# Kernel tuning notes

Measured on AMD Instinct MI355X. Metric: run time of the kernel, lower is better.

Reference implementation:

```python
import jax, jax.numpy as jnp
import numpy as np

DIM_IN = 1024
DIM_OUT = 1024


def setup_inputs() -> dict:
    key = jax.random.key(0)
    k1, k2, k3, k4 = jax.random.split(key, 4)
    X = jax.random.normal(k1, (4, 2048, DIM_IN), dtype=jnp.float32)
    s = 1.0 / np.sqrt(DIM_IN)
    Wq = jax.random.normal(k2, (DIM_IN, DIM_OUT), dtype=jnp.float32) * s
    Wk = jax.random.normal(k3, (DIM_IN, DIM_OUT), dtype=jnp.float32) * s
    Wv = jax.random.normal(k4, (DIM_IN, DIM_OUT), dtype=jnp.float32) * s
    return {"X": X, "Wq": Wq, "Wk": Wk, "Wv": Wv}


def reference(X, Wq, Wk, Wv):
    # X: [B, T, Din]; projections (qkv_bias=False)
    q = jnp.einsum('btd,de->bte', X, Wq)   # [B, T, Dout]
    k = jnp.einsum('btd,de->bte', X, Wk)
    v = jnp.einsum('btd,de->bte', X, Wv)
    T = X.shape[1]
    scores = jnp.einsum('bqe,bke->bqk', q, k)  # [B, T, T]
    causal = jnp.tril(jnp.ones((T, T), dtype=bool))  # mask upper triangle (future)
    scores = jnp.where(causal, scores, -jnp.inf)
    # scale=True: divide by sqrt(d); -inf stays -inf so order vs mask is irrelevant
    scores = scores / jnp.sqrt(jnp.asarray(k.shape[-1], dtype=scores.dtype))
    weights = jax.nn.softmax(scores, axis=-1)
    # dropout p=0.0 -> identity
    return jnp.einsum('bqk,bke->bqe', weights, v)
```

## Files before the change

### kernel.cpp

```cpp
#include <hip/hip_runtime.h>
#include <hip/hip_bf16.h>

typedef unsigned short u16;
typedef __bf16 bf16x8 __attribute__((ext_vector_type(8)));
typedef float f32x4 __attribute__((ext_vector_type(4)));
typedef unsigned short u16x8 __attribute__((ext_vector_type(8)));
typedef unsigned short u16x4 __attribute__((ext_vector_type(4)));

__device__ __forceinline__ float bf2f(u16 u) {
  unsigned int x = ((unsigned int)u) << 16;
  return __builtin_bit_cast(float, x);
}
__device__ __forceinline__ u16 f2bf(float f) {
  unsigned int x = __builtin_bit_cast(unsigned int, f);
  x = x + 0x7FFFu + ((x >> 16) & 1u);
  return (u16)(x >> 16);
}

__device__ __forceinline__ void gload_lds16(const u16* g, u16* l) {
  __builtin_amdgcn_global_load_lds(
      (const __attribute__((address_space(1))) unsigned int*)(unsigned long long)(uintptr_t)g,
      (__attribute__((address_space(3))) unsigned int*)(unsigned int)(uintptr_t)l,
      16, 0, 0);
}

__global__ __launch_bounds__(256) void prep_kernel(const float* __restrict__ X,
                                                   const float* __restrict__ Wq,
                                                   const float* __restrict__ Wk,
                                                   const float* __restrict__ Wv,
                                                   u16* __restrict__ Xb,
                                                   u16* __restrict__ Wt) {
  const int id = blockIdx.x;
  const int tid = threadIdx.x;
  if (id < 4096) {
    long i = ((long)id * 256 + tid) * 8;
    float4 a = *reinterpret_cast<const float4*>(X + i);
    float4 b = *reinterpret_cast<const float4*>(X + i + 4);
    u16x8 o;
    o[0] = f2bf(a.x); o[1] = f2bf(a.y); o[2] = f2bf(a.z); o[3] = f2bf(a.w);
    o[4] = f2bf(b.x); o[5] = f2bf(b.y); o[6] = f2bf(b.z); o[7] = f2bf(b.w);
    *reinterpret_cast<u16x8*>(Xb + i) = o;
    return;
  }
  __shared__ u16 t[64][72];
  const int id2 = id - 4096;
  const int z = id2 >> 8;
  const float* W = (z == 0) ? Wq : (z == 1) ? Wk : Wv;
  const float scale = (z == 0) ? (1.0f / 32.0f) : 1.0f;
  u16* out = Wt + (long)z * 1048576;
  const int c0 = (id2 & 15) * 64;
  const int r0 = ((id2 >> 4) & 15) * 64;
#pragma unroll
  for (int i = 0; i < 4; ++i) {
    int slot = tid + 256 * i;
    int lr = slot >> 4;
    int lc4 = slot & 15;
    float4 v = *reinterpret_cast<const float4*>(W + (long)(r0 + lr) * 1024 + c0 + lc4 * 4);
    t[lr][lc4 * 4 + 0] = f2bf(v.x * scale);
    t[lr][lc4 * 4 + 1] = f2bf(v.y * scale);
    t[lr][lc4 * 4 + 2] = f2bf(v.z * scale);
    t[lr][lc4 * 4 + 3] = f2bf(v.w * scale);
  }
  __syncthreads();
#pragma unroll
  for (int i = 0; i < 2; ++i) {
    int slot = tid + 256 * i;
    int orow = slot >> 3;
    int oc = slot & 7;
    u16x8 o;
#pragma unroll
    for (int j = 0; j < 8; ++j) o[j] = t[oc * 8 + j][orow];
    *reinterpret_cast<u16x8*>(out + (long)(c0 + orow) * 1024 + r0 + oc * 8) = o;
  }
}

__global__ __launch_bounds__(512, 4) void gemm_qkv(const u16* __restrict__ Xb,
                                                   const u16* __restrict__ Wt,
                                                   u16* __restrict__ Qb,
                                                   u16* __restrict__ Vt) {
  const int id = blockIdx.x;
  const int xcd = id & 7, j = id >> 3;
  const int bn = (xcd & 1) * 8 + (j & 7);
  const int bm = ((xcd >> 1) << 4) + (j >> 3);
  const int m0 = bm * 128, n0 = bn * 192;
  const int K = 1024;

  __shared__ u16 ldsA[2][8192];
  __shared__ u16 ldsB[2][12288];

  const int tid = threadIdx.x;
  const int lane = tid & 63;
  const int wid = tid >> 6;
  const int wm = wid >> 2, wn = wid & 3;
  const int l16 = lane & 15, lh = lane >> 4;
  const int strow = tid >> 3;
  const int scol = ((tid & 7) ^ (strow & 7)) * 8;
  const int rsw = l16 & 7;

  f32x4 acc[4][3];
#pragma unroll
  for (int mi = 0; mi < 4; ++mi)
#pragma unroll
    for (int ni = 0; ni < 3; ++ni) acc[mi][ni] = (f32x4)(0.0f);

  auto stage = [&](int d, int k0) {
#pragma unroll
    for (int l = 0; l < 2; ++l)
      gload_lds16(Xb + (long)(m0 + l * 64 + strow) * K + k0 + scol,
                  &ldsA[d][l * 4096 + tid * 8]);
#pragma unroll
    for (int l = 0; l < 3; ++l)
      gload_lds16(Wt + (long)(n0 + l * 64 + strow) * K + k0 + scol,
                  &ldsB[d][l * 4096 + tid * 8]);
  };

  stage(0, 0);
  int cur = 0;
  for (int k0 = 0; k0 < K; k0 += 64) {
    __syncthreads();
    if (k0 + 64 < K) stage(cur ^ 1, k0 + 64);
#pragma unroll
    for (int kk = 0; kk < 2; ++kk) {
      bf16x8 af[4], bfr[3];
#pragma unroll
      for (int mi = 0; mi < 4; ++mi)
        af[mi] = *reinterpret_cast<const bf16x8*>(
            &ldsA[cur][(wm * 64 + mi * 16 + l16) * 64 + (((kk * 4 + lh) ^ rsw)) * 8]);
#pragma unroll
      for (int ni = 0; ni < 3; ++ni)
        bfr[ni] = *reinterpret_cast<const bf16x8*>(
            &ldsB[cur][(wn * 48 + ni * 16 + l16) * 64 + (((kk * 4 + lh) ^ rsw)) * 8]);
#pragma unroll
      for (int mi = 0; mi < 4; ++mi)
#pragma unroll
        for (int ni = 0; ni < 3; ++ni)
          acc[mi][ni] = __builtin_amdgcn_mfma_f32_16x16x32_bf16(bfr[ni], af[mi], acc[mi][ni], 0, 0, 0);
    }
    cur ^= 1;
  }

  const int rowt = m0 + wm * 64 + l16;
#pragma unroll
  for (int ni = 0; ni < 3; ++ni) {
    const int gc0 = n0 + wn * 48 + ni * 16 + lh * 4;
    const int z = gc0 >> 10;
    const int lc = gc0 & 1023;
    if (z < 2) {
      u16* C = Qb + (long)z * 8388608;
#pragma unroll
      for (int mi = 0; mi < 4; ++mi) {
        u16x4 o;
#pragma unroll
        for (int r = 0; r < 4; ++r) o[r] = f2bf(acc[mi][ni][r]);
        *reinterpret_cast<u16x4*>(&C[(long)(rowt + mi * 16) * 1024 + lc]) = o;
      }
    } else {
#pragma unroll
      for (int mi = 0; mi < 4; ++mi) {
        const int grow = rowt + mi * 16;
        const int b = grow >> 11, t = grow & 2047;
#pragma unroll
        for (int r = 0; r < 4; ++r)
          Vt[(long)b * 2097152 + (long)(lc + r) * 2048 + t] = f2bf(acc[mi][ni][r]);
      }
    }
  }
}

__global__ __launch_bounds__(256, 3) void gemm_s(const u16* __restrict__ Qb,
                                                 const u16* __restrict__ Kb,
                                                 u16* __restrict__ Sg,
                                                 float* __restrict__ Sums) {
  const int id = blockIdx.x;
  const int x = id & 7;
  const int q = id >> 3;
  const int bz = q / 34;
  int u = q - bz * 34;
  int qr, kc;
  const int n1 = 32 - 2 * x;
  if (u < n1) { kc = x;      qr = 2 * x + u; }
  else        { kc = 15 - x; qr = 30 - 2 * x + (u - n1); }
  const int m0 = qr * 64, n0 = kc * 128;
  const int K = 1024;

  const u16* A = Qb + (long)bz * 2097152;
  const u16* B = Kb + (long)bz * 2097152;

  __shared__ u16 ldsA[2][4096];
  __shared__ u16 ldsB[2][8192];

  const int tid = threadIdx.x;
  const int lane = tid & 63;
  const int wn = tid >> 6;
  const int l16 = lane & 15, lh = lane >> 4;
  const int strow = tid >> 3;
  const int scol = ((tid & 7) ^ (strow & 7)) * 8;
  const int rsw = l16 & 7;

  f32x4 acc[4][2];
#pragma unroll
  for (int mi = 0; mi < 4; ++mi)
#pragma unroll
    for (int ni = 0; ni < 2; ++ni) acc[mi][ni] = (f32x4)(0.0f);

  auto stage = [&](int d, int k0) {
#pragma unroll
    for (int l = 0; l < 2; ++l)
      gload_lds16(A + (long)(m0 + l * 32 + strow) * K + k0 + scol,
                  &ldsA[d][l * 2048 + tid * 8]);
#pragma unroll
    for (int l = 0; l < 4; ++l)
      gload_lds16(B + (long)(n0 + l * 32 + strow) * K + k0 + scol,
                  &ldsB[d][l * 2048 + tid * 8]);
  };

  stage(0, 0);
  int cur = 0;
  for (int k0 = 0; k0 < K; k0 += 64) {
    __syncthreads();
    if (k0 + 64 < K) stage(cur ^ 1, k0 + 64);
#pragma unroll
    for (int kk = 0; kk < 2; ++kk) {
      bf16x8 af[4], bfr[2];
#pragma unroll
      for (int mi = 0; mi < 4; ++mi)
        af[mi] = *reinterpret_cast<const bf16x8*>(
            &ldsA[cur][(mi * 16 + l16) * 64 + (((kk * 4 + lh) ^ rsw)) * 8]);
#pragma unroll
      for (int ni = 0; ni < 2; ++ni)
        bfr[ni] = *reinterpret_cast<const bf16x8*>(
            &ldsB[cur][(wn * 32 + ni * 16 + l16) * 64 + (((kk * 4 + lh) ^ rsw)) * 8]);
#pragma unroll
      for (int mi = 0; mi < 4; ++mi)
#pragma unroll
        for (int ni = 0; ni < 2; ++ni)
          acc[mi][ni] = __builtin_amdgcn_mfma_f32_16x16x32_bf16(bfr[ni], af[mi], acc[mi][ni], 0, 0, 0);
    }
    cur ^= 1;
  }

  u16* C = Sg + (long)bz * 4194304;
  float* sums = Sums + (long)bz * 2048;
  const int coln = n0 + wn * 32 + lh * 4;
#pragma unroll
  for (int mi = 0; mi < 4; ++mi) {
    const int gr = m0 + mi * 16 + l16;
    float rs = 0.0f;
#pragma unroll
    for (int ni = 0; ni < 2; ++ni) {
      u16x4 o;
#pragma unroll
      for (int r = 0; r < 4; ++r) {
        const int gc = coln + ni * 16 + r;
        const float e = (gc <= gr) ? __expf(acc[mi][ni][r]) : 0.0f;
        const u16 ub = f2bf(e);
        o[r] = ub;
        rs += bf2f(ub);
      }
      *reinterpret_cast<u16x4*>(&C[(long)gr * 2048 + coln + ni * 16]) = o;
    }
    rs += __shfl_xor(rs, 16);
    rs += __shfl_xor(rs, 32);
    if (lh == 0) atomicAdd(&sums[gr], rs);
  }
}

__global__ __launch_bounds__(512, 2) void gemm_pv(const u16* __restrict__ Ag,
                                                  const u16* __restrict__ Bg,
                                                  float* __restrict__ Cg,
                                                  const float* __restrict__ Sums) {
  const int id = blockIdx.x;
  const int x = id & 7;
  const int q = id >> 3;
  const int f = (q ^ (q >> 5)) & 1;
  const int i5 = ((q >> 1) & 15) | (((q >> 5) & 1) << 4);
  const int bmb = i5 & 7;
  const int bz = (i5 >> 3) & 3;
  const int bm = f ? (15 - bmb) : bmb;
  const int bn = x;
  const int K = 2048;

  const u16* A = Ag + (long)bz * 4194304;
  const u16* B = Bg + (long)bz * 2097152;
  const int m0 = bm * 128, n0 = bn * 128;
  const int kEnd = m0 + 128;

  __shared__ u16 ldsA[2][8192];
  __shared__ u16 ldsB[2][8192];

  const int tid = threadIdx.x;
  const int lane = tid & 63;
  const int wid = tid >> 6;
  const int wm = wid >> 2, wn = wid & 3;
  const int l16 = lane & 15, lh = lane >> 4;
  const int strow = tid >> 3;
  const int scol = ((tid & 7) ^ (strow & 7)) * 8;
  const int rsw = l16 & 7;

  f32x4 acc[4][2];
#pragma unroll
  for (int mi = 0; mi < 4; ++mi)
#pragma unroll
    for (int ni = 0; ni < 2; ++ni) acc[mi][ni] = (f32x4)(0.0f);

  auto stage = [&](int d, int k0) {
#pragma unroll
    for (int l = 0; l < 2; ++l) {
      const int row = l * 64 + strow;
      gload_lds16(A + (long)(m0 + row) * K + k0 + scol, &ldsA[d][l * 4096 + tid * 8]);
      gload_lds16(B + (long)(n0 + row) * K + k0 + scol, &ldsB[d][l * 4096 + tid * 8]);
    }
  };

  stage(0, 0);
  int cur = 0;
  for (int k0 = 0; k0 < kEnd; k0 += 64) {
    __syncthreads();
    if (k0 + 64 < kEnd) stage(cur ^ 1, k0 + 64);
#pragma unroll
    for (int kk = 0; kk < 2; ++kk) {
      bf16x8 af[4], bfr[2];
#pragma unroll
      for (int mi = 0; mi < 4; ++mi)
        af[mi] = *reinterpret_cast<const bf16x8*>(
            &ldsA[cur][(wm * 64 + mi * 16 + l16) * 64 + (((kk * 4 + lh) ^ rsw)) * 8]);
#pragma unroll
      for (int ni = 0; ni < 2; ++ni)
        bfr[ni] = *reinterpret_cast<const bf16x8*>(
            &ldsB[cur][(wn * 32 + ni * 16 + l16) * 64 + (((kk * 4 + lh) ^ rsw)) * 8]);
#pragma unroll
      for (int mi = 0; mi < 4; ++mi)
#pragma unroll
        for (int ni = 0; ni < 2; ++ni)
          acc[mi][ni] = __builtin_amdgcn_mfma_f32_16x16x32_bf16(bfr[ni], af[mi], acc[mi][ni], 0, 0, 0);
    }
    cur ^= 1;
  }

  float* C = Cg + (long)bz * 2097152;
  const float* sums = Sums + (long)bz * 2048;
  const long rown = (long)(m0 + wm * 64 + l16);
  const int coln = n0 + wn * 32 + lh * 4;
#pragma unroll
  for (int mi = 0; mi < 4; ++mi) {
    const float inv = 1.0f / sums[(int)rown + mi * 16];
#pragma unroll
    for (int ni = 0; ni < 2; ++ni) {
      f32x4 v = acc[mi][ni] * inv;
      *reinterpret_cast<f32x4*>(&C[(rown + mi * 16) * 1024 + coln + ni * 16]) = v;
    }
  }
}

extern "C" void kernel_launch(void* const* d_in, const int* in_sizes, int n_in,
                              void* d_out, int out_size, void* d_ws, size_t ws_size,
                              hipStream_t stream) {
  const float* X  = (const float*)d_in[0];
  const float* Wq = (const float*)d_in[1];
  const float* Wk = (const float*)d_in[2];
  const float* Wv = (const float*)d_in[3];

  u16* Xb = (u16*)d_ws;
  u16* Wt = Xb + 8388608;
  u16* Qb = Wt + 3145728;
  u16* Kb = Qb + 8388608;
  u16* Vt = Kb + 8388608;
  u16* S  = Vt + 8388608;
  float* sums = (float*)(S + 16777216);

  hipMemsetAsync(sums, 0, 4 * 2048 * sizeof(float), stream);

  prep_kernel<<<4864, 256, 0, stream>>>(X, Wq, Wk, Wv, Xb, Wt);

  gemm_qkv<<<1024, 512, 0, stream>>>(Xb, Wt, Qb, Vt);

  gemm_s<<<1088, 256, 0, stream>>>(Qb, Kb, S, sums);

  gemm_pv<<<512, 512, 0, stream>>>(S, Vt, (float*)d_out, sums);
}
```

Baseline: 132.3 us.

## Precompute Wq·Wk^T to fold K projection into a single fused weight

Computes G = Wq·Wk^T once per call with a small GEMM, then projects X through [G | Wv] so scores become (X·G)·X^T and no separate K tensor is needed. This removes a third of the projection GEMM work and the K write. The projection GEMM is retiled to 128x128 with 256-thread blocks and templated for both uses. It adds an extra launch and an extra bf16 rounding of G, which can change numerical error.

```diff
diff --git a/kernel.cpp b/kernel.cpp
--- a/kernel.cpp
+++ b/kernel.cpp
@@ -29,37 +29,50 @@
                                                    const float* __restrict__ Wk,
                                                    const float* __restrict__ Wv,
                                                    u16* __restrict__ Xb,
-                                                   u16* __restrict__ Wt) {
+                                                   u16* __restrict__ Wqr,
+                                                   u16* __restrict__ Wkr,
+                                                   u16* __restrict__ WG) {
   const int id = blockIdx.x;
   const int tid = threadIdx.x;
-  if (id < 4096) {
-    long i = ((long)id * 256 + tid) * 8;
-    float4 a = *reinterpret_cast<const float4*>(X + i);
-    float4 b = *reinterpret_cast<const float4*>(X + i + 4);
+  if (id < 5120) {
+    const float* src;
+    u16* dst;
+    float scale = 1.0f;
+    long i;
+    if (id < 4096) {
+      src = X; dst = Xb; i = ((long)id * 256 + tid) * 8;
+    } else if (id < 4608) {
+      src = Wq; dst = Wqr; scale = 1.0f / 32.0f;
+      i = ((long)(id - 4096) * 256 + tid) * 8;
+    } else {
+      src = Wk; dst = Wkr;
+      i = ((long)(id - 4608) * 256 + tid) * 8;
+    }
+    float4 a = *reinterpret_cast<const float4*>(src + i);
+    float4 b = *reinterpret_cast<const float4*>(src + i + 4);
     u16x8 o;
-    o[0] = f2bf(a.x); o[1] = f2bf(a.y); o[2] = f2bf(a.z); o[3] = f2bf(a.w);
-    o[4] = f2bf(b.x); o[5] = f2bf(b.y); o[6] = f2bf(b.z); o[7] = f2bf(b.w);
-    *reinterpret_cast<u16x8*>(Xb + i) = o;
+    o[0] = f2bf(a.x * scale); o[1] = f2bf(a.y * scale);
+    o[2] = f2bf(a.z * scale); o[3] = f2bf(a.w * scale);
+    o[4] = f2bf(b.x * scale); o[5] = f2bf(b.y * scale);
+    o[6] = f2bf(b.z * scale); o[7] = f2bf(b.w * scale);
+    *reinterpret_cast<u16x8*>(dst + i) = o;
     return;
   }
   __shared__ u16 t[64][72];
-  const int id2 = id - 4096;
-  const int z = id2 >> 8;
-  const float* W = (z == 0) ? Wq : (z == 1) ? Wk : Wv;
-  const float scale = (z == 0) ? (1.0f / 32.0f) : 1.0f;
-  u16* out = Wt + (long)z * 1048576;
+  const int id2 = id - 5120;
+  u16* out = WG + 1048576;
   const int c0 = (id2 & 15) * 64;
-  const int r0 = ((id2 >> 4) & 15) * 64;
+  const int r0 = (id2 >> 4) * 64;
 #pragma unroll
   for (int i = 0; i < 4; ++i) {
     int slot = tid + 256 * i;
     int lr = slot >> 4;
     int lc4 = slot & 15;
-    float4 v = *reinterpret_cast<const float4*>(W + (long)(r0 + lr) * 1024 + c0 + lc4 * 4);
-    t[lr][lc4 * 4 + 0] = f2bf(v.x * scale);
-    t[lr][lc4 * 4 + 1] = f2bf(v.y * scale);
-    t[lr][lc4 * 4 + 2] = f2bf(v.z * scale);
-    t[lr][lc4 * 4 + 3] = f2bf(v.w * scale);
+    float4 v = *reinterpret_cast<const float4*>(Wv + (long)(r0 + lr) * 1024 + c0 + lc4 * 4);
+    t[lr][lc4 * 4 + 0] = f2bf(v.x);
+    t[lr][lc4 * 4 + 1] = f2bf(v.y);
+    t[lr][lc4 * 4 + 2] = f2bf(v.z);
+    t[lr][lc4 * 4 + 3] = f2bf(v.w);
   }
   __syncthreads();
 #pragma unroll
@@ -74,44 +87,53 @@
   }
 }
 
-__global__ __launch_bounds__(512, 4) void gemm_qkv(const u16* __restrict__ Xb,
-                                                   const u16* __restrict__ Wt,
-                                                   u16* __restrict__ Qb,
-                                                   u16* __restrict__ Vt) {
-  const int id = blockIdx.x;
-  const int xcd = id & 7, j = id >> 3;
-  const int bn = (xcd & 1) * 8 + (j & 7);
-  const int bm = ((xcd >> 1) << 4) + (j >> 3);
-  const int m0 = bm * 128, n0 = bn * 192;
+template <int MODE>
+__global__ __launch_bounds__(256, 2) void gemm128(const u16* __restrict__ A,
+                                                  const u16* __restrict__ B,
+                                                  u16* __restrict__ C,
+                                                  u16* __restrict__ Vt) {
+  int bm, bn;
+  if constexpr (MODE == 0) {
+    bm = blockIdx.x >> 3;
+    bn = blockIdx.x & 7;
+  } else {
+    const int id = blockIdx.x;
+    const int xcd = id & 7, j = id >> 3;
+    bn = (xcd & 1) * 8 + (j & 7);
+    bm = ((xcd >> 1) << 4) + (j >> 3);
+  }
+  const int m0 = bm * 128, n0 = bn * 128;
   const int K = 1024;
 
+  bool vblk = false;
+  if constexpr (MODE == 1) vblk = (bn >> 3) == 1;
+
   __shared__ u16 ldsA[2][8192];
-  __shared__ u16 ldsB[2][12288];
+  __shared__ u16 ldsB[2][8192];
 
   const int tid = threadIdx.x;
   const int lane = tid & 63;
   const int wid = tid >> 6;
-  const int wm = wid >> 2, wn = wid & 3;
+  const int wm = wid >> 1, wn = wid & 1;
   const int l16 = lane & 15, lh = lane >> 4;
-  const int strow = tid >> 3;
-  const int scol = ((tid & 7) ^ (strow & 7)) * 8;
+  const int srow = lane >> 3;
+  const int scol = ((lane & 7) ^ srow) * 8;
   const int rsw = l16 & 7;
 
-  f32x4 acc[4][3];
+  f32x4 acc[4][4];
 #pragma unroll
   for (int mi = 0; mi < 4; ++mi)
 #pragma unroll
-    for (int ni = 0; ni < 3; ++ni) acc[mi][ni] = (f32x4)(0.0f);
+    for (int ni = 0; ni < 4; ++ni) acc[mi][ni] = (f32x4)(0.0f);
 
   auto stage = [&](int d, int k0) {
 #pragma unroll
-    for (int l = 0; l < 2; ++l)
-      gload_lds16(Xb + (long)(m0 + l * 64 + strow) * K + k0 + scol,
-                  &ldsA[d][l * 4096 + tid * 8]);
-#pragma unroll
-    for (int l = 0; l < 3; ++l)
-      gload_lds16(Wt + (long)(n0 + l * 64 + strow) * K + k0 + scol,
-                  &ldsB[d][l * 4096 + tid * 8]);
+    for (int s = 0; s < 4; ++s) {
+      const int seg = wid * 4 + s;
+      const int row = seg * 8 + srow;
+      gload_lds16(A + (long)(m0 + row) * K + k0 + scol, &ldsA[d][seg * 512]);
+      gload_lds16(B + (long)(n0 + row) * K + k0 + scol, &ldsB[d][seg * 512]);
+    }
   };
 
   stage(0, 0);
@@ -121,54 +143,64 @@
     if (k0 + 64 < K) stage(cur ^ 1, k0 + 64);
 #pragma unroll
     for (int kk = 0; kk < 2; ++kk) {
-      bf16x8 af[4], bfr[3];
+      bf16x8 af[4], bfr[4];
 #pragma unroll
       for (int mi = 0; mi < 4; ++mi)
         af[mi] = *reinterpret_cast<const bf16x8*>(
             &ldsA[cur][(wm * 64 + mi * 16 + l16) * 64 + (((kk * 4 + lh) ^ rsw)) * 8]);
 #pragma unroll
-      for (int ni = 0; ni < 3; ++ni)
+      for (int ni = 0; ni < 4; ++ni)
         bfr[ni] = *reinterpret_cast<const bf16x8*>(
-            &ldsB[cur][(wn * 48 + ni * 16 + l16) * 64 + (((kk * 4 + lh) ^ rsw)) * 8]);
-#pragma unroll
-      for (int mi = 0; mi < 4; ++mi)
-#pragma unroll
-        for (int ni = 0; ni < 3; ++ni)
-          acc[mi][ni] = __builtin_amdgcn_mfma_f32_16x16x32_bf16(bfr[ni], af[mi], acc[mi][ni], 0, 0, 0);
+            &ldsB[cur][(wn * 64 + ni * 16 + l16) * 64 + (((kk * 4 + lh) ^ rsw)) * 8]);
+      if (!vblk) {
+#pragma unroll
+        for (int mi = 0; mi < 4; ++mi)
+#pragma unroll
+          for (int ni = 0; ni < 4; ++ni)
+            acc[mi][ni] = __builtin_amdgcn_mfma_f32_16x16x32_bf16(bfr[ni], af[mi], acc[mi][ni], 0, 0, 0);
+      } else {
+#pragma unroll
+        for (int mi = 0; mi < 4; ++mi)
+#pragma unroll
+          for (int ni = 0; ni < 4; ++ni)
+            acc[mi][ni] = __builtin_amdgcn_mfma_f32_16x16x32_bf16(af[mi], bfr[ni], acc[mi][ni], 0, 0, 0);
+      }
     }
     cur ^= 1;
   }
 
-  const int rowt = m0 + wm * 64 + l16;
-#pragma unroll
-  for (int ni = 0; ni < 3; ++ni) {
-    const int gc0 = n0 + wn * 48 + ni * 16 + lh * 4;
-    const int z = gc0 >> 10;
-    const int lc = gc0 & 1023;
-    if (z < 2) {
-      u16* C = Qb + (long)z * 8388608;
-#pragma unroll
-      for (int mi = 0; mi < 4; ++mi) {
+  if (!vblk) {
+    const int col0 = (MODE == 0) ? n0 : (bn & 7) * 128;
+    const long rown = (long)(m0 + wm * 64 + l16);
+    const int coln = col0 + wn * 64 + lh * 4;
+#pragma unroll
+    for (int mi = 0; mi < 4; ++mi)
+#pragma unroll
+      for (int ni = 0; ni < 4; ++ni) {
         u16x4 o;
 #pragma unroll
         for (int r = 0; r < 4; ++r) o[r] = f2bf(acc[mi][ni][r]);
-        *reinterpret_cast<u16x4*>(&C[(long)(rowt + mi * 16) * 1024 + lc]) = o;
+        *reinterpret_cast<u16x4*>(&C[(rown + mi * 16) * 1024 + coln + ni * 16]) = o;
       }
-    } else {
-#pragma unroll
-      for (int mi = 0; mi < 4; ++mi) {
-        const int grow = rowt + mi * 16;
-        const int b = grow >> 11, t = grow & 2047;
-#pragma unroll
-        for (int r = 0; r < 4; ++r)
-          Vt[(long)b * 2097152 + (long)(lc + r) * 2048 + t] = f2bf(acc[mi][ni][r]);
+  } else {
+    const int b = m0 >> 11;
+    const int t0 = (m0 & 2047) + wm * 64 + lh * 4;
+    const int e0 = (bn & 7) * 128 + wn * 64 + l16;
+#pragma unroll
+    for (int mi = 0; mi < 4; ++mi)
+#pragma unroll
+      for (int ni = 0; ni < 4; ++ni) {
+        u16x4 o;
+#pragma unroll
+        for (int r = 0; r < 4; ++r) o[r] = f2bf(acc[mi][ni][r]);
+        *reinterpret_cast<u16x4*>(
+            &Vt[(long)b * 2097152 + (long)(e0 + ni * 16) * 2048 + t0 + mi * 16]) = o;
       }
-    }
-  }
-}
-
-__global__ __launch_bounds__(256, 3) void gemm_s(const u16* __restrict__ Qb,
-                                                 const u16* __restrict__ Kb,
+  }
+}
+
+__global__ __launch_bounds__(256, 3) void gemm_s(const u16* __restrict__ T1,
+                                                 const u16* __restrict__ Xb,
                                                  u16* __restrict__ Sg,
                                                  float* __restrict__ Sums) {
   const int id = blockIdx.x;
@@ -183,8 +215,8 @@
   const int m0 = qr * 64, n0 = kc * 128;
   const int K = 1024;
 
-  const u16* A = Qb + (long)bz * 2097152;
-  const u16* B = Kb + (long)bz * 2097152;
+  const u16* A = T1 + (long)bz * 2097152;
+  const u16* B = Xb + (long)bz * 2097152;
 
   __shared__ u16 ldsA[2][4096];
   __shared__ u16 ldsB[2][8192];
@@ -360,21 +392,24 @@
   const float* Wk = (const float*)d_in[2];
   const float* Wv = (const float*)d_in[3];
 
-  u16* Xb = (u16*)d_ws;
-  u16* Wt = Xb + 8388608;
-  u16* Qb = Wt + 3145728;
-  u16* Kb = Qb + 8388608;
-  u16* Vt = Kb + 8388608;
-  u16* S  = Vt + 8388608;
+  u16* Xb  = (u16*)d_ws;
+  u16* Wqr = Xb + 8388608;
+  u16* Wkr = Wqr + 1048576;
+  u16* WG  = Wkr + 1048576;
+  u16* T1  = WG + 2097152;
+  u16* Vt  = T1 + 8388608;
+  u16* S   = Vt + 8388608;
   float* sums = (float*)(S + 16777216);
 
   hipMemsetAsync(sums, 0, 4 * 2048 * sizeof(float), stream);
 
-  prep_kernel<<<4864, 256, 0, stream>>>(X, Wq, Wk, Wv, Xb, Wt);
-
-  gemm_qkv<<<1024, 512, 0, stream>>>(Xb, Wt, Qb, Vt);
-
-  gemm_s<<<1088, 256, 0, stream>>>(Qb, Kb, S, sums);
+  prep_kernel<<<5376, 256, 0, stream>>>(X, Wq, Wk, Wv, Xb, Wqr, Wkr, WG);
+
+  gemm128<0><<<64, 256, 0, stream>>>(Wkr, Wqr, WG, nullptr);
+
+  gemm128<1><<<1024, 256, 0, stream>>>(Xb, WG, T1, Vt);
+
+  gemm_s<<<1088, 256, 0, stream>>>(T1, Xb, S, sums);
 
   gemm_pv<<<512, 512, 0, stream>>>(S, Vt, (float*)d_out, sums);
 }
```

Result: no change. 134.8 us (+2.0%).
